# Kernel tuning notes

Measured on AMD Instinct MI355X. Metric: run time of the kernel, lower is better.

The kernel has to match this reference:

```python
import jax, jax.numpy as jnp
import numpy as np

FRAME_LENGTH = 512
HOP_LENGTH = 256
ENERGY_THRESHOLD = 0.01
SAMPLE_RATE = 16000
SILENCE_FRAMES = int(0.3 * SAMPLE_RATE / HOP_LENGTH)      # 18
MIN_SPEECH_FRAMES = int(0.1 * SAMPLE_RATE / HOP_LENGTH)   # 6


def setup_inputs() -> dict:
    key = jax.random.key(0)
    waveform = jax.random.normal(key, (32, 960000), dtype=jnp.float32)
    return {"waveform": waveform}


def _compute_energy(waveform):
    # (B, S) -> (B, T): short-time mean-square energy, full frames only
    n = waveform.shape[-1]
    num_frames = max(1, (n - FRAME_LENGTH) // HOP_LENGTH + 1)
    idx = jnp.arange(num_frames)[:, None] * HOP_LENGTH + jnp.arange(FRAME_LENGTH)[None, :]
    frames = waveform[:, idx]                     # (B, T, F)
    return jnp.mean(frames * frames, axis=-1)


def _threshold(e):
    # torch.quantile(non_zero, 0.2) with linear interpolation; fallback to fixed threshold
    n = e.shape[0]
    s = jnp.sort(e)
    nzero = jnp.sum(s <= 0)          # number of entries excluded by (> 0)
    nz = n - nzero                   # count of positive entries
    pos = 0.2 * (nz - 1).astype(jnp.float32)
    lo = jnp.floor(pos).astype(jnp.int32)
    hi = jnp.ceil(pos).astype(jnp.int32)
    frac = pos - lo.astype(jnp.float32)
    ilo = jnp.clip(nzero + lo, 0, n - 1)
    ihi = jnp.clip(nzero + hi, 0, n - 1)
    q = s[ilo] * (1.0 - frac) + s[ihi] * frac
    return jnp.where(nz > 0, q, jnp.float32(ENERGY_THRESHOLD))


def _vad_one(e):
    # Faithful scan-based version of the per-frame hysteresis state machine.
    n = e.shape[0]
    m = e > _threshold(e)

    def step(state, xs):
        in_sp, start, sil = state
        t, mt = xs
        start2 = jnp.where(mt & ~in_sp, t, start)
        sil2 = jnp.where(mt, jnp.int32(0), jnp.where(in_sp, sil + 1, sil))
        closed = (~mt) & in_sp & (sil2 >= SILENCE_FRAMES)
        end = t - sil2  # matches original: end = t - silence_count (exclusive)
        in_sp2 = jnp.where(mt, True, jnp.where(closed, False, in_sp))
        return (in_sp2, start2, sil2), (closed, start2, end)

    init = (jnp.bool_(False), jnp.int32(0), jnp.int32(0))
    (in_sp_f, start_f, _), (closed, starts, ends) = jax.lax.scan(
        step, init, (jnp.arange(n, dtype=jnp.int32), m))

    # trailing open segment -> (start, n)
    starts = jnp.concatenate([starts, start_f[None]])
    ends = jnp.concatenate([ends, jnp.full((1,), n, dtype=jnp.int32)])
    valid = jnp.concatenate([closed, in_sp_f[None]])
    valid = valid & ((ends - starts) >= MIN_SPEECH_FRAMES)

    # mark mask[start:end] = True via +1/-1 diff then cumsum (RLE)
    sentinel = n + 1
    idx_s = jnp.where(valid, jnp.clip(starts, 0, n), sentinel)
    idx_e = jnp.where(valid, jnp.clip(ends, 0, n), sentinel)
    d = jnp.zeros(n + 2, dtype=jnp.int32)
    d = d.at[idx_s].add(1).at[idx_e].add(-1)
    return jnp.cumsum(d)[:n] > 0


def reference(waveform):
    energy = _compute_energy(waveform)     # (B, T)
    return jax.vmap(_vad_one)(energy)      # (B, T) bool VAD mask
```

## Files before the change

kernel.cpp:

```cpp
#include <hip/hip_runtime.h>

#define NFRAMES 3749
#define NBLOCKS 3750
#define NSAMP   960000
#define NBATCH  32
#define NWORDS  59
#define SILENCE_FRAMES 18
#define MIN_SPEECH_FRAMES 6
#define MAXSEG  256

__global__ __launch_bounds__(256) void vad_block_sums(const float* __restrict__ wav,
                                                      double* __restrict__ bs) {
    int tid = threadIdx.x;
    const float* p = wav + (size_t)blockIdx.x * 4096 + tid * 16;
    double acc = 0.0;
    #pragma unroll
    for (int i = 0; i < 4; ++i) {
        float4 v = *(const float4*)(p + i * 4);
        acc += (double)(v.x * v.x);
        acc += (double)(v.y * v.y);
        acc += (double)(v.z * v.z);
        acc += (double)(v.w * v.w);
    }
    #pragma unroll
    for (int m = 1; m < 16; m <<= 1)
        acc += __shfl_xor(acc, m, 64);
    if ((tid & 15) == 0)
        bs[(size_t)blockIdx.x * 16 + (tid >> 4)] = acc;
}

__global__ __launch_bounds__(256) void vad_finish(const double* __restrict__ bs,
                                                  int* __restrict__ out) {
    __shared__ float eng[NFRAMES];
    __shared__ int hist4[4][256];
    __shared__ unsigned long long mw[NWORDS];
    __shared__ unsigned long long sw[NWORDS];
    __shared__ unsigned long long lw[NWORDS];
    __shared__ unsigned long long Sw[NWORDS];
    __shared__ unsigned long long Ew[NWORDS];
    __shared__ int wbS[NWORDS], wbL[NWORDS];
    __shared__ int startpos[MAXSEG], lastpos[MAXSEG];
    __shared__ int nzero_sh, nseg_sh;
    __shared__ unsigned sel_prefix_sh;
    __shared__ int sel_k_sh;
    __shared__ int cLE_sh;
    __shared__ unsigned minGT_sh;
    __shared__ float thr_sh;

    int b = blockIdx.x;
    int tid = threadIdx.x;
    int lane = tid & 63, wv = tid >> 6;
    const double* row = bs + (size_t)b * NBLOCKS;

    if (tid == 0) nzero_sh = 0;
    __syncthreads();

    unsigned ub[15];
    int nel = 0, myzero = 0;
    #pragma unroll
    for (int i = 0; i < 15; ++i) {
        int t = tid + (i << 8);
        if (t < NFRAMES) {
            double s = row[t] + row[t + 1];
            float e = (float)(s * (1.0 / 512.0));
            eng[t] = e;
            ub[nel++] = __float_as_uint(e);
            if (e <= 0.0f) myzero++;
        }
    }
    if (myzero) atomicAdd(&nzero_sh, myzero);
    __syncthreads();

    int nzero = nzero_sh;
    int nz = NFRAMES - nzero;

    if (nz > 0) {
        float pos = 0.2f * (float)(nz - 1);
        int lo = (int)floorf(pos), hi = (int)ceilf(pos);
        int rank_lo = min(max(nzero + lo, 0), NFRAMES - 1);
        int rank_hi = min(max(nzero + hi, 0), NFRAMES - 1);

        for (int i = tid; i < 1024; i += 256) ((int*)hist4)[i] = 0;
        if (tid == 0) { sel_prefix_sh = 0u; sel_k_sh = rank_lo; }
        __syncthreads();

        for (int shift = 24; shift >= 0; shift -= 8) {
            unsigned pref = sel_prefix_sh;
            unsigned pmask = (shift == 24) ? 0u : (0xFFFFFFFFu << (shift + 8));
            for (int j = 0; j < nel; ++j) {
                unsigned u = ub[j];
                if ((u & pmask) == (pref & pmask))
                    atomicAdd(&hist4[wv][(u >> shift) & 255], 1);
            }
            __syncthreads();
            if (wv == 0) {
                int bin0 = lane << 2;
                int4 h0 = *(const int4*)&hist4[0][bin0];
                int4 h1 = *(const int4*)&hist4[1][bin0];
                int4 h2 = *(const int4*)&hist4[2][bin0];
                int4 h3 = *(const int4*)&hist4[3][bin0];
                int h[4];
                h[0] = h0.x + h1.x + h2.x + h3.x;
                h[1] = h0.y + h1.y + h2.y + h3.y;
                h[2] = h0.z + h1.z + h2.z + h3.z;
                h[3] = h0.w + h1.w + h2.w + h3.w;
                int tot = h[0] + h[1] + h[2] + h[3];
                int inc = tot;
                #pragma unroll
                for (int off = 1; off < 64; off <<= 1) {
                    int y = __shfl_up(inc, off, 64);
                    if (lane >= off) inc += y;
                }
                int run = inc - tot;
                int k = sel_k_sh;
                #pragma unroll
                for (int j = 0; j < 4; ++j) {
                    if (k >= run && k < run + h[j]) {
                        sel_prefix_sh = pref | ((unsigned)(bin0 + j) << shift);
                        sel_k_sh = k - run;
                    }
                    run += h[j];
                }
            }
            __syncthreads();
            if (shift > 0) {
                for (int i = tid; i < 1024; i += 256) ((int*)hist4)[i] = 0;
            }
            __syncthreads();
        }

        unsigned vb = sel_prefix_sh;

        if (rank_hi != rank_lo) {
            if (tid == 0) { cLE_sh = 0; minGT_sh = 0xFFFFFFFFu; }
            __syncthreads();
            int c = 0;
            unsigned mg = 0xFFFFFFFFu;
            for (int j = 0; j < nel; ++j) {
                unsigned u = ub[j];
                if (u <= vb) c++;
                else mg = min(mg, u);
            }
            #pragma unroll
            for (int off = 32; off > 0; off >>= 1) {
                c += __shfl_xor(c, off, 64);
                mg = min(mg, (unsigned)__shfl_xor((int)mg, off, 64));
            }
            if (lane == 0) {
                atomicAdd(&cLE_sh, c);
                atomicMin(&minGT_sh, mg);
            }
            __syncthreads();
        }

        if (tid == 0) {
            float vlo = __uint_as_float(vb);
            float vhi;
            if (rank_hi == rank_lo) vhi = vlo;
            else vhi = (cLE_sh >= rank_lo + 2) ? vlo : __uint_as_float(minGT_sh);
            float frac = pos - (float)lo;
            thr_sh = vlo * (1.0f - frac) + vhi * frac;
        }
    } else {
        if (tid == 0) thr_sh = 0.01f;
    }
    __syncthreads();
    float thr = thr_sh;

    for (int wi = wv; wi < NWORDS; wi += 4) {
        int t = (wi << 6) + lane;
        bool p = (t < NFRAMES) && (eng[t] > thr);
        unsigned long long bm = __ballot(p);
        if (lane == 0) mw[wi] = bm;
    }
    __syncthreads();

    for (int wi = wv; wi < NWORDS; wi += 4) {
        unsigned long long W  = mw[wi];
        unsigned long long Wm = (wi > 0) ? mw[wi - 1] : 0ull;
        unsigned long long Wp = (wi + 1 < NWORDS) ? mw[wi + 1] : 0ull;
        int l = lane;
        bool mt = (W >> l) & 1ull;
        bool prev_any, next_any;
        if (l >= 18) {
            prev_any = ((W >> (l - 18)) & 0x3FFFFull) != 0ull;
        } else {
            unsigned long long lowpart = W & ((1ull << l) - 1ull);
            unsigned long long hipart  = Wm >> (46 + l);
            prev_any = (lowpart | hipart) != 0ull;
        }
        if (l <= 45) {
            next_any = ((W >> (l + 1)) & 0x3FFFFull) != 0ull;
        } else {
            unsigned long long a  = (l < 63) ? (W >> (l + 1)) : 0ull;
            unsigned long long bb = Wp & ((1ull << (l - 45)) - 1ull);
            next_any = (a | bb) != 0ull;
        }
        unsigned long long bS = __ballot(mt && !prev_any);
        unsigned long long bL = __ballot(mt && !next_any);
        if (lane == 0) { sw[wi] = bS; lw[wi] = bL; }
    }
    __syncthreads();

    if (tid < NWORDS) {
        int cS = 0, cL = 0;
        for (int j = 0; j < tid; ++j) { cS += __popcll(sw[j]); cL += __popcll(lw[j]); }
        wbS[tid] = cS; wbL[tid] = cL;
        if (tid == NWORDS - 1) nseg_sh = cS + __popcll(sw[tid]);
    }
    __syncthreads();

    for (int wi = wv; wi < NWORDS; wi += 4) {
        unsigned long long wS = sw[wi], wL = lw[wi];
        int t = (wi << 6) + lane;
        unsigned long long lmask = (1ull << lane) - 1ull;
        if ((wS >> lane) & 1ull) startpos[wbS[wi] + __popcll(wS & lmask)] = t;
        if ((wL >> lane) & 1ull) lastpos[wbL[wi] + __popcll(wL & lmask)] = t;
    }
    for (int wi = tid; wi < NWORDS; wi += 256) { Sw[wi] = 0ull; Ew[wi] = 0ull; }
    __syncthreads();

    int nseg = nseg_sh;
    for (int k = tid; k < nseg; k += 256) {
        int s = startpos[k], L = lastpos[k];
        int e = (L >= NFRAMES - SILENCE_FRAMES) ? NFRAMES : L;
        if (e - s >= MIN_SPEECH_FRAMES) {
            atomicOr(&Sw[s >> 6], 1ull << (s & 63));
            atomicOr(&Ew[e >> 6], 1ull << (e & 63));
        }
    }
    __syncthreads();

    if (tid < NWORDS) {
        int cS = 0, cE = 0;
        for (int j = 0; j < tid; ++j) { cS += __popcll(Sw[j]); cE += __popcll(Ew[j]); }
        wbS[tid] = cS; wbL[tid] = cE;
    }
    __syncthreads();

    int* orow = out + (size_t)b * NFRAMES;
    for (int wi = wv; wi < NWORDS; wi += 4) {
        unsigned long long wS2 = Sw[wi], wE2 = Ew[wi];
        int t = (wi << 6) + lane;
        unsigned long long ile = (lane == 63) ? ~0ull : ((1ull << (lane + 1)) - 1ull);
        int cS = wbS[wi] + __popcll(wS2 & ile);
        int cE = wbL[wi] + __popcll(wE2 & ile);
        if (t < NFRAMES) orow[t] = (cS > cE) ? 1 : 0;
    }
}

extern "C" void kernel_launch(void* const* d_in, const int* in_sizes, int n_in,
                              void* d_out, int out_size, void* d_ws, size_t ws_size,
                              hipStream_t stream) {
    const float* wav = (const float*)d_in[0];
    int* out = (int*)d_out;
    double* bs = (double*)d_ws;

    vad_block_sums<<<(NBATCH * NSAMP) / 4096, 256, 0, stream>>>(wav, bs);
    vad_finish<<<NBATCH, 256, 0, stream>>>(bs, out);
}
```

Measured before the change: 195.9 us.

## Replace atomic radix-histogram selection with 2-bit radix counting via wave reductions

Rewrites the quantile selection in the finish kernel. Shared-memory atomic 8-bit histograms are replaced by 16 passes of 2-bit digit counting, using register counters and wavefront shuffle reductions, with fewer barriers per pass. The block grows to 512 threads, energies stay in registers instead of a shared array, and the serial per-word prefix loops become wave scans. This trades 4 passes for 16 passes, each cheaper, to cut atomic contention and synchronisation in the latency-bound 32-block tail kernel.

After: 203.6 us. 3.9% more time.

```diff
diff --git a/kernel.cpp b/kernel.cpp
--- a/kernel.cpp
+++ b/kernel.cpp
@@ -8,6 +8,7 @@
 #define SILENCE_FRAMES 18
 #define MIN_SPEECH_FRAMES 6
 #define MAXSEG  256
+#define NT      512
 
 __global__ __launch_bounds__(256) void vad_block_sums(const float* __restrict__ wav,
                                                       double* __restrict__ bs) {
@@ -29,10 +30,8 @@
         bs[(size_t)blockIdx.x * 16 + (tid >> 4)] = acc;
 }
 
-__global__ __launch_bounds__(256) void vad_finish(const double* __restrict__ bs,
-                                                  int* __restrict__ out) {
-    __shared__ float eng[NFRAMES];
-    __shared__ int hist4[4][256];
+__global__ __launch_bounds__(NT) void vad_finish(const double* __restrict__ bs,
+                                                 int* __restrict__ out) {
     __shared__ unsigned long long mw[NWORDS];
     __shared__ unsigned long long sw[NWORDS];
     __shared__ unsigned long long lw[NWORDS];
@@ -40,142 +39,132 @@
     __shared__ unsigned long long Ew[NWORDS];
     __shared__ int wbS[NWORDS], wbL[NWORDS];
     __shared__ int startpos[MAXSEG], lastpos[MAXSEG];
-    __shared__ int nzero_sh, nseg_sh;
-    __shared__ unsigned sel_prefix_sh;
-    __shared__ int sel_k_sh;
-    __shared__ int cLE_sh;
-    __shared__ unsigned minGT_sh;
-    __shared__ float thr_sh;
+    __shared__ int zc[8];
+    __shared__ int r01[2][8], r2[2][8];
+    __shared__ int cle[8];
+    __shared__ unsigned mgt[8];
+    __shared__ int nseg_sh;
 
     int b = blockIdx.x;
     int tid = threadIdx.x;
     int lane = tid & 63, wv = tid >> 6;
     const double* row = bs + (size_t)b * NBLOCKS;
 
-    if (tid == 0) nzero_sh = 0;
-    __syncthreads();
-
-    unsigned ub[15];
+    unsigned ub[8];
     int nel = 0, myzero = 0;
     #pragma unroll
-    for (int i = 0; i < 15; ++i) {
-        int t = tid + (i << 8);
+    for (int i = 0; i < 8; ++i) {
+        int t = tid + (i << 9);
         if (t < NFRAMES) {
             double s = row[t] + row[t + 1];
             float e = (float)(s * (1.0 / 512.0));
-            eng[t] = e;
-            ub[nel++] = __float_as_uint(e);
-            if (e <= 0.0f) myzero++;
-        }
-    }
-    if (myzero) atomicAdd(&nzero_sh, myzero);
-    __syncthreads();
-
-    int nzero = nzero_sh;
+            ub[i] = __float_as_uint(e);
+            ++nel;
+            if (e <= 0.0f) ++myzero;
+        } else {
+            ub[i] = 0u;
+        }
+    }
+    int z = myzero;
+    #pragma unroll
+    for (int off = 32; off; off >>= 1) z += __shfl_xor(z, off, 64);
+    if (lane == 0) zc[wv] = z;
+    __syncthreads();
+    int nzero = 0;
+    #pragma unroll
+    for (int i = 0; i < 8; ++i) nzero += zc[i];
     int nz = NFRAMES - nzero;
 
+    float thr;
     if (nz > 0) {
         float pos = 0.2f * (float)(nz - 1);
         int lo = (int)floorf(pos), hi = (int)ceilf(pos);
         int rank_lo = min(max(nzero + lo, 0), NFRAMES - 1);
         int rank_hi = min(max(nzero + hi, 0), NFRAMES - 1);
 
-        for (int i = tid; i < 1024; i += 256) ((int*)hist4)[i] = 0;
-        if (tid == 0) { sel_prefix_sh = 0u; sel_k_sh = rank_lo; }
-        __syncthreads();
-
-        for (int shift = 24; shift >= 0; shift -= 8) {
-            unsigned pref = sel_prefix_sh;
-            unsigned pmask = (shift == 24) ? 0u : (0xFFFFFFFFu << (shift + 8));
+        unsigned base = 0u;
+        int k = rank_lo;
+        for (int step = 15; step >= 0; --step) {
+            int shift = step << 1;
+            int par = step & 1;
+            int c0 = 0, c1 = 0, c2 = 0;
             for (int j = 0; j < nel; ++j) {
                 unsigned u = ub[j];
-                if ((u & pmask) == (pref & pmask))
-                    atomicAdd(&hist4[wv][(u >> shift) & 255], 1);
-            }
+                bool match = (((u ^ base) >> shift) >> 2) == 0u;
+                unsigned d = (u >> shift) & 3u;
+                if (match) {
+                    c0 += (d == 0u);
+                    c1 += (d == 1u);
+                    c2 += (d == 2u);
+                }
+            }
+            int p01 = c0 | (c1 << 16);
+            #pragma unroll
+            for (int off = 32; off; off >>= 1) {
+                p01 += __shfl_xor(p01, off, 64);
+                c2  += __shfl_xor(c2, off, 64);
+            }
+            if (lane == 0) { r01[par][wv] = p01; r2[par][wv] = c2; }
             __syncthreads();
-            if (wv == 0) {
-                int bin0 = lane << 2;
-                int4 h0 = *(const int4*)&hist4[0][bin0];
-                int4 h1 = *(const int4*)&hist4[1][bin0];
-                int4 h2 = *(const int4*)&hist4[2][bin0];
-                int4 h3 = *(const int4*)&hist4[3][bin0];
-                int h[4];
-                h[0] = h0.x + h1.x + h2.x + h3.x;
-                h[1] = h0.y + h1.y + h2.y + h3.y;
-                h[2] = h0.z + h1.z + h2.z + h3.z;
-                h[3] = h0.w + h1.w + h2.w + h3.w;
-                int tot = h[0] + h[1] + h[2] + h[3];
-                int inc = tot;
-                #pragma unroll
-                for (int off = 1; off < 64; off <<= 1) {
-                    int y = __shfl_up(inc, off, 64);
-                    if (lane >= off) inc += y;
-                }
-                int run = inc - tot;
-                int k = sel_k_sh;
-                #pragma unroll
-                for (int j = 0; j < 4; ++j) {
-                    if (k >= run && k < run + h[j]) {
-                        sel_prefix_sh = pref | ((unsigned)(bin0 + j) << shift);
-                        sel_k_sh = k - run;
-                    }
-                    run += h[j];
-                }
-            }
-            __syncthreads();
-            if (shift > 0) {
-                for (int i = tid; i < 1024; i += 256) ((int*)hist4)[i] = 0;
-            }
-            __syncthreads();
-        }
-
-        unsigned vb = sel_prefix_sh;
+            int C0 = 0, C1 = 0, C2 = 0;
+            #pragma unroll
+            for (int i = 0; i < 8; ++i) {
+                int v = r01[par][i];
+                C0 += v & 0xFFFF;
+                C1 += v >> 16;
+                C2 += r2[par][i];
+            }
+            unsigned d;
+            if (k < C0)                 { d = 0u; }
+            else if (k < C0 + C1)       { d = 1u; k -= C0; }
+            else if (k < C0 + C1 + C2)  { d = 2u; k -= C0 + C1; }
+            else                        { d = 3u; k -= C0 + C1 + C2; }
+            base |= d << shift;
+        }
+        unsigned vb = base;
+        float vlo = __uint_as_float(vb), vhi;
 
         if (rank_hi != rank_lo) {
-            if (tid == 0) { cLE_sh = 0; minGT_sh = 0xFFFFFFFFu; }
-            __syncthreads();
             int c = 0;
             unsigned mg = 0xFFFFFFFFu;
             for (int j = 0; j < nel; ++j) {
                 unsigned u = ub[j];
-                if (u <= vb) c++;
+                if (u <= vb) ++c;
                 else mg = min(mg, u);
             }
             #pragma unroll
-            for (int off = 32; off > 0; off >>= 1) {
+            for (int off = 32; off; off >>= 1) {
                 c += __shfl_xor(c, off, 64);
-                mg = min(mg, (unsigned)__shfl_xor((int)mg, off, 64));
-            }
-            if (lane == 0) {
-                atomicAdd(&cLE_sh, c);
-                atomicMin(&minGT_sh, mg);
-            }
+                unsigned o = (unsigned)__shfl_xor((int)mg, off, 64);
+                mg = min(mg, o);
+            }
+            if (lane == 0) { cle[wv] = c; mgt[wv] = mg; }
             __syncthreads();
-        }
-
-        if (tid == 0) {
-            float vlo = __uint_as_float(vb);
-            float vhi;
-            if (rank_hi == rank_lo) vhi = vlo;
-            else vhi = (cLE_sh >= rank_lo + 2) ? vlo : __uint_as_float(minGT_sh);
-            float frac = pos - (float)lo;
-            thr_sh = vlo * (1.0f - frac) + vhi * frac;
-        }
+            int C = 0;
+            unsigned MG = 0xFFFFFFFFu;
+            #pragma unroll
+            for (int i = 0; i < 8; ++i) { C += cle[i]; MG = min(MG, mgt[i]); }
+            vhi = (C >= rank_lo + 2) ? vlo : __uint_as_float(MG);
+        } else {
+            vhi = vlo;
+        }
+        float frac = pos - (float)lo;
+        thr = vlo * (1.0f - frac) + vhi * frac;
     } else {
-        if (tid == 0) thr_sh = 0.01f;
-    }
-    __syncthreads();
-    float thr = thr_sh;
-
-    for (int wi = wv; wi < NWORDS; wi += 4) {
-        int t = (wi << 6) + lane;
-        bool p = (t < NFRAMES) && (eng[t] > thr);
+        thr = 0.01f;
+    }
+
+    #pragma unroll
+    for (int i = 0; i < 8; ++i) {
+        int t = tid + (i << 9);
+        bool p = (t < NFRAMES) && (__uint_as_float(ub[i]) > thr);
         unsigned long long bm = __ballot(p);
-        if (lane == 0) mw[wi] = bm;
-    }
-    __syncthreads();
-
-    for (int wi = wv; wi < NWORDS; wi += 4) {
+        int w = (i << 3) + wv;
+        if (lane == 0 && w < NWORDS) mw[w] = bm;
+    }
+    __syncthreads();
+
+    for (int wi = wv; wi < NWORDS; wi += 8) {
         unsigned long long W  = mw[wi];
         unsigned long long Wm = (wi > 0) ? mw[wi - 1] : 0ull;
         unsigned long long Wp = (wi + 1 < NWORDS) ? mw[wi + 1] : 0ull;
@@ -202,27 +191,35 @@
     }
     __syncthreads();
 
-    if (tid < NWORDS) {
-        int cS = 0, cL = 0;
-        for (int j = 0; j < tid; ++j) { cS += __popcll(sw[j]); cL += __popcll(lw[j]); }
-        wbS[tid] = cS; wbL[tid] = cL;
-        if (tid == NWORDS - 1) nseg_sh = cS + __popcll(sw[tid]);
-    }
-    __syncthreads();
-
-    for (int wi = wv; wi < NWORDS; wi += 4) {
+    if (tid < 64) {
+        unsigned long long wS = (tid < NWORDS) ? sw[tid] : 0ull;
+        unsigned long long wL = (tid < NWORDS) ? lw[tid] : 0ull;
+        int pS = __popcll(wS), pL = __popcll(wL);
+        int iS = pS, iL = pL;
+        #pragma unroll
+        for (int off = 1; off < 64; off <<= 1) {
+            int a = __shfl_up(iS, off, 64);
+            int c = __shfl_up(iL, off, 64);
+            if (lane >= off) { iS += a; iL += c; }
+        }
+        if (tid < NWORDS) { wbS[tid] = iS - pS; wbL[tid] = iL - pL; }
+        if (tid == 63) nseg_sh = iS;
+    }
+    __syncthreads();
+
+    for (int wi = wv; wi < NWORDS; wi += 8) {
         unsigned long long wS = sw[wi], wL = lw[wi];
         int t = (wi << 6) + lane;
         unsigned long long lmask = (1ull << lane) - 1ull;
         if ((wS >> lane) & 1ull) startpos[wbS[wi] + __popcll(wS & lmask)] = t;
         if ((wL >> lane) & 1ull) lastpos[wbL[wi] + __popcll(wL & lmask)] = t;
     }
-    for (int wi = tid; wi < NWORDS; wi += 256) { Sw[wi] = 0ull; Ew[wi] = 0ull; }
+    for (int wi = tid; wi < NWORDS; wi += NT) { Sw[wi] = 0ull; Ew[wi] = 0ull; }
     __syncthreads();
 
     int nseg = nseg_sh;
-    for (int k = tid; k < nseg; k += 256) {
-        int s = startpos[k], L = lastpos[k];
+    for (int k2 = tid; k2 < nseg; k2 += NT) {
+        int s = startpos[k2], L = lastpos[k2];
         int e = (L >= NFRAMES - SILENCE_FRAMES) ? NFRAMES : L;
         if (e - s >= MIN_SPEECH_FRAMES) {
             atomicOr(&Sw[s >> 6], 1ull << (s & 63));
@@ -231,15 +228,23 @@
     }
     __syncthreads();
 
-    if (tid < NWORDS) {
-        int cS = 0, cE = 0;
-        for (int j = 0; j < tid; ++j) { cS += __popcll(Sw[j]); cE += __popcll(Ew[j]); }
-        wbS[tid] = cS; wbL[tid] = cE;
+    if (tid < 64) {
+        unsigned long long wS = (tid < NWORDS) ? Sw[tid] : 0ull;
+        unsigned long long wE = (tid < NWORDS) ? Ew[tid] : 0ull;
+        int pS = __popcll(wS), pE = __popcll(wE);
+        int iS = pS, iE = pE;
+        #pragma unroll
+        for (int off = 1; off < 64; off <<= 1) {
+            int a = __shfl_up(iS, off, 64);
+            int c = __shfl_up(iE, off, 64);
+            if (lane >= off) { iS += a; iE += c; }
+        }
+        if (tid < NWORDS) { wbS[tid] = iS - pS; wbL[tid] = iE - pE; }
     }
     __syncthreads();
 
     int* orow = out + (size_t)b * NFRAMES;
-    for (int wi = wv; wi < NWORDS; wi += 4) {
+    for (int wi = wv; wi < NWORDS; wi += 8) {
         unsigned long long wS2 = Sw[wi], wE2 = Ew[wi];
         int t = (wi << 6) + lane;
         unsigned long long ile = (lane == 63) ? ~0ull : ((1ull << (lane + 1)) - 1ull);
@@ -257,5 +262,5 @@
     double* bs = (double*)d_ws;
 
     vad_block_sums<<<(NBATCH * NSAMP) / 4096, 256, 0, stream>>>(wav, bs);
-    vad_finish<<<NBATCH, 256, 0, stream>>>(bs, out);
+    vad_finish<<<NBATCH, NT, 0, stream>>>(bs, out);
 }
```
